# Kernel tuning notes

Measured on AMD Instinct MI355X. Metric: run time of the kernel, lower is better.

Reference implementation:

```python
import jax, jax.numpy as jnp
import numpy as np

B, L, H, NH, D, I = 2, 2048, 2048, 16, 128, 8192
EPS = 1e-6
ROPE_BASE = 10000.0


def rms_norm(x, w):
    x32 = x.astype(jnp.float32)
    n = x32 * jax.lax.rsqrt(jnp.mean(x32 * x32, axis=-1, keepdims=True) + EPS)
    return (n * w).astype(x.dtype)


def rope(x, offset):
    # x: [B, L, H, D], non-traditional (half-split) RoPE
    d = x.shape[-1]
    half = d // 2
    inv_freq = 1.0 / (ROPE_BASE ** (jnp.arange(half, dtype=jnp.float32) * 2.0 / d))
    pos = jnp.arange(x.shape[1], dtype=jnp.float32) + offset
    ang = pos[:, None] * inv_freq[None, :]              # [L, half]
    cos = jnp.cos(ang)[None, :, None, :]
    sin = jnp.sin(ang)[None, :, None, :]
    x1, x2 = x[..., :half], x[..., half:]
    out = jnp.concatenate([x1 * cos - x2 * sin, x2 * cos + x1 * sin], axis=-1)
    return out.astype(x.dtype)


def setup_inputs() -> dict:
    key = jax.random.key(0)
    ks = jax.random.split(key, 9)
    s = 0.02
    causal = jnp.where(jnp.tril(jnp.ones((L, L), dtype=bool)), 0.0, -1e9).astype(jnp.float32)
    return {
        "x": jax.random.normal(ks[0], (B, L, H), dtype=jnp.float32),
        "ln1_w": jnp.ones((H,), dtype=jnp.float32),
        "ln2_w": jnp.ones((H,), dtype=jnp.float32),
        "wq": jax.random.normal(ks[1], (H, H), dtype=jnp.float32) * s,
        "wk": jax.random.normal(ks[2], (H, H), dtype=jnp.float32) * s,
        "wv": jax.random.normal(ks[3], (H, H), dtype=jnp.float32) * s,
        "wo": jax.random.normal(ks[4], (H, H), dtype=jnp.float32) * s,
        "w_gate": jax.random.normal(ks[5], (I, H), dtype=jnp.float32) * s,
        "w_up": jax.random.normal(ks[6], (I, H), dtype=jnp.float32) * s,
        "w_down": jax.random.normal(ks[7], (H, I), dtype=jnp.float32) * s,
        "mask": causal,
        "offset": 0,
    }


def reference(x, ln1_w, ln2_w, wq, wk, wv, wo, w_gate, w_up, w_down, mask, offset):
    residual = x
    h = rms_norm(x, ln1_w)
    # QKV projections (torch Linear: y = x @ W.T)
    q = jnp.einsum("ble,oe->blo", h, wq).reshape(B, L, NH, D)
    k = jnp.einsum("ble,oe->blo", h, wk).reshape(B, L, NH, D)
    v = jnp.einsum("ble,oe->blo", h, wv).reshape(B, L, NH, D)
    q = rope(q, offset)
    k = rope(k, offset)
    # [B, NH, L, D]
    q = q.transpose(0, 2, 1, 3)
    k = k.transpose(0, 2, 1, 3)
    v = v.transpose(0, 2, 1, 3)
    scores = jnp.einsum("bhqd,bhkd->bhqk", q.astype(jnp.float32), k.astype(jnp.float32))
    scores = scores / np.sqrt(D).astype(np.float32)
    if mask is not None:
        scores = scores + mask
    probs = jax.nn.softmax(scores, axis=-1).astype(v.dtype)
    attn = jnp.einsum("bhqk,bhkd->bhqd", probs, v)
    attn = attn.transpose(0, 2, 1, 3).reshape(B, L, NH * D)
    h = jnp.einsum("blo,eo->ble", attn, wo)
    x = h + residual
    residual = x
    h = rms_norm(x, ln2_w)
    gate = jax.nn.silu(jnp.einsum("ble,ie->bli", h, w_gate))
    up = jnp.einsum("ble,ie->bli", h, w_up)
    mlp = jnp.einsum("bli,ei->ble", gate * up, w_down)
    return mlp + residual
```

## Files before the change

kernel.cpp:

```cpp
#include <hip/hip_runtime.h>
#include <stdint.h>

#define B_ 2
#define L_ 2048
#define H_ 2048
#define NH_ 16
#define D_ 128
#define I_ 8192
#define M_ (B_*L_)

typedef unsigned short u16;
typedef __attribute__((ext_vector_type(8))) short bf16x8;
typedef __attribute__((ext_vector_type(4))) float f32x4;

__device__ __forceinline__ u16 f2bf(float f) {
  union { float f; uint32_t u; } c; c.f = f;
  return (u16)((c.u + 0x7fffu + ((c.u >> 16) & 1u)) >> 16);
}
__device__ __forceinline__ float bf2f(u16 h) {
  union { uint32_t u; float f; } c; c.u = ((uint32_t)h) << 16;
  return c.f;
}
__device__ __forceinline__ void gload16(const void* g, void* l) {
  __builtin_amdgcn_global_load_lds(
      (__attribute__((address_space(1))) void*)g,
      (__attribute__((address_space(3))) void*)l, 16, 0, 0);
}

__global__ void cvt_w(const float* __restrict__ src, u16* __restrict__ dst, int n4) {
  int i = blockIdx.x * blockDim.x + threadIdx.x;
  if (i >= n4) return;
  float4 v = ((const float4*)src)[i];
  ushort4 o;
  o.x = f2bf(v.x); o.y = f2bf(v.y); o.z = f2bf(v.z); o.w = f2bf(v.w);
  ((ushort4*)dst)[i] = o;
}

__global__ __launch_bounds__(256) void rmsnorm_k(const float* __restrict__ x,
                                                 const float* __restrict__ w,
                                                 u16* __restrict__ out) {
  int row = blockIdx.x;
  int t = threadIdx.x;
  const float4* xr = (const float4*)(x + (size_t)row * H_);
  float4 a = xr[t * 2], b = xr[t * 2 + 1];
  float s = a.x*a.x + a.y*a.y + a.z*a.z + a.w*a.w
          + b.x*b.x + b.y*b.y + b.z*b.z + b.w*b.w;
  for (int m = 1; m < 64; m <<= 1) s += __shfl_xor(s, m);
  __shared__ float sm[4];
  if ((t & 63) == 0) sm[t >> 6] = s;
  __syncthreads();
  float tot = sm[0] + sm[1] + sm[2] + sm[3];
  float rs = rsqrtf(tot / (float)H_ + 1e-6f);
  const float4* wr = (const float4*)w;
  float4 w0 = wr[t * 2], w1 = wr[t * 2 + 1];
  ushort4 o0, o1;
  o0.x = f2bf(a.x * rs * w0.x); o0.y = f2bf(a.y * rs * w0.y);
  o0.z = f2bf(a.z * rs * w0.z); o0.w = f2bf(a.w * rs * w0.w);
  o1.x = f2bf(b.x * rs * w1.x); o1.y = f2bf(b.y * rs * w1.y);
  o1.z = f2bf(b.z * rs * w1.z); o1.w = f2bf(b.w * rs * w1.w);
  ushort4* orow = (ushort4*)(out + (size_t)row * H_);
  orow[t * 2] = o0; orow[t * 2 + 1] = o1;
}

__global__ void rope_tab(float* __restrict__ cosT, float* __restrict__ sinT,
                         const int* __restrict__ offp) {
  int i = blockIdx.x * blockDim.x + threadIdx.x;
  int d = i & 63, l = i >> 6;
  float inv = powf(10000.0f, -(float)d / 64.0f);
  float ang = (float)(l + *offp) * inv;
  cosT[i] = cosf(ang);
  sinT[i] = sinf(ang);
}

__global__ void rope_apply(u16* __restrict__ qk, const float* __restrict__ cosT,
                           const float* __restrict__ sinT) {
  int i = blockIdx.x * blockDim.x + threadIdx.x;
  int d = i & 63;
  size_t row = (size_t)(i >> 6);
  int l = (int)(row & (L_ - 1));
  u16* p = qk + row * D_;
  float x1 = bf2f(p[d]), x2 = bf2f(p[d + 64]);
  float c = cosT[l * 64 + d], s = sinT[l * 64 + d];
  p[d]      = f2bf(x1 * c - x2 * s);
  p[d + 64] = f2bf(x2 * c + x1 * s);
}

__global__ __launch_bounds__(256) void vtrans_k(const u16* __restrict__ v,
                                                u16* __restrict__ vt) {
  __shared__ u16 tile[64][65];
  int l0 = blockIdx.x * 64, d0 = blockIdx.y * 64;
  size_t base = (size_t)blockIdx.z * L_ * D_;
  int t = threadIdx.x;
  int tr = t >> 3, tc = (t & 7) * 8;
  #pragma unroll
  for (int it = 0; it < 2; ++it) {
    int r = tr + it * 32;
    const u16* src = v + base + (size_t)(l0 + r) * D_ + d0 + tc;
    ushort4 u0 = ((const ushort4*)src)[0], u1 = ((const ushort4*)src)[1];
    tile[r][tc + 0] = u0.x; tile[r][tc + 1] = u0.y;
    tile[r][tc + 2] = u0.z; tile[r][tc + 3] = u0.w;
    tile[r][tc + 4] = u1.x; tile[r][tc + 5] = u1.y;
    tile[r][tc + 6] = u1.z; tile[r][tc + 7] = u1.w;
  }
  __syncthreads();
  #pragma unroll
  for (int it = 0; it < 2; ++it) {
    int r = tr + it * 32;
    u16* dst = vt + base + (size_t)(d0 + r) * L_ + l0 + tc;
    ushort4 o0, o1;
    o0.x = tile[tc + 0][r]; o0.y = tile[tc + 1][r];
    o0.z = tile[tc + 2][r]; o0.w = tile[tc + 3][r];
    o1.x = tile[tc + 4][r]; o1.y = tile[tc + 5][r];
    o1.z = tile[tc + 6][r]; o1.w = tile[tc + 7][r];
    ((ushort4*)dst)[0] = o0; ((ushort4*)dst)[1] = o1;
  }
}

#define EPI_QKV 0
#define EPI_SILU 1
#define EPI_MUL 2
#define EPI_ADDRES 3

template <int EPI>
__global__ __launch_bounds__(256)
void gemm_bt(const u16* __restrict__ A, const u16* __restrict__ Bw,
             int M, int N, int K,
             u16* outb, float* outf, const float* __restrict__ resf) {
  __shared__ __attribute__((aligned(16))) u16 At[128 * 64];
  __shared__ __attribute__((aligned(16))) u16 Bt[128 * 64];
  int tid = threadIdx.x;
  int w = tid >> 6, lane = tid & 63;
  int r16 = lane & 15, g4 = lane >> 4;
  int wr = w >> 1, wc = w & 1;
  int m0 = blockIdx.y * 128;
  int n0 = blockIdx.x * 128;
  f32x4 acc[4][4] = {};
  const char* Ab = (const char*)A;
  const char* Bb = (const char*)Bw;
  int nk = K >> 6;
  for (int kt = 0; kt < nk; ++kt) {
    int k0 = kt << 6;
    #pragma unroll
    for (int i = 0; i < 4; ++i) {
      int uoff = i * 4096 + w * 1024;
      int lin = uoff + lane * 16;
      int row = lin >> 7;
      int colB = lin & 127;
      gload16(Ab + ((size_t)(m0 + row) * K + k0) * 2 + colB, (char*)At + uoff);
      gload16(Bb + ((size_t)(n0 + row) * K + k0) * 2 + colB, (char*)Bt + uoff);
    }
    __syncthreads();
    #pragma unroll
    for (int kk = 0; kk < 2; ++kk) {
      bf16x8 af[4], bfr[4];
      #pragma unroll
      for (int m = 0; m < 4; ++m)
        af[m] = *(const bf16x8*)&At[(wr * 64 + m * 16 + r16) * 64 + kk * 32 + g4 * 8];
      #pragma unroll
      for (int n = 0; n < 4; ++n)
        bfr[n] = *(const bf16x8*)&Bt[(wc * 64 + n * 16 + r16) * 64 + kk * 32 + g4 * 8];
      #pragma unroll
      for (int m = 0; m < 4; ++m)
        #pragma unroll
        for (int n = 0; n < 4; ++n)
          acc[m][n] = __builtin_amdgcn_mfma_f32_16x16x32_bf16(af[m], bfr[n], acc[m][n], 0, 0, 0);
    }
    __syncthreads();
  }
  #pragma unroll
  for (int m = 0; m < 4; ++m) {
    #pragma unroll
    for (int n = 0; n < 4; ++n) {
      #pragma unroll
      for (int r = 0; r < 4; ++r) {
        int row = m0 + wr * 64 + m * 16 + g4 * 4 + r;
        int col = n0 + wc * 64 + n * 16 + r16;
        float val = acc[m][n][r];
        if (EPI == EPI_QKV) {
          int b = row >> 11, l = row & 2047;
          int hh = col >> 7, d = col & 127;
          outb[((((size_t)b * NH_ + hh) * L_ + l) << 7) + d] = f2bf(val);
        } else if (EPI == EPI_SILU) {
          float sg = val / (1.0f + __expf(-val));
          outb[(size_t)row * N + col] = f2bf(sg);
        } else if (EPI == EPI_MUL) {
          float g = bf2f(outb[(size_t)row * N + col]);
          outb[(size_t)row * N + col] = f2bf(g * val);
        } else {
          outf[(size_t)row * N + col] = val + resf[(size_t)row * N + col];
        }
      }
    }
  }
}

template <int EPI>
__global__ __launch_bounds__(512, 2)
void gemm256(const u16* __restrict__ A, const u16* __restrict__ Bw,
             int M, int N, int K, u16* __restrict__ outb) {
  __shared__ __attribute__((aligned(16))) u16 Asm[2][2][8192];
  __shared__ __attribute__((aligned(16))) u16 Bsm[2][2][8192];
  int tid = threadIdx.x;
  int wid = tid >> 6, lane = tid & 63;
  int r16 = lane & 15, g4 = lane >> 4;
  int nwg = gridDim.x, bid = blockIdx.x;
  int q8 = nwg >> 3, r8 = nwg & 7, xcd = bid & 7, loc = bid >> 3;
  int wg = (xcd < r8 ? xcd * (q8 + 1) : r8 * (q8 + 1) + (xcd - r8) * q8) + loc;
  int NX = N >> 8;
  int n0 = (wg % NX) * 256;
  int m0 = (wg / NX) * 256;
  const char* Ab = (const char*)A;
  const char* Bb = (const char*)Bw;
  int nk = K >> 6;

  f32x4 acc[2][2][4][2] = {};
  bf16x8 afr[4][2];
  bf16x8 bfr[2][2][2];

  auto STAGE = [&](int kt1, int sel) {
    if (kt1 >= nk) return;
    int buf = kt1 & 1;
    int k0 = kt1 << 6;
    const char* gb; char* lb; int row0;
    if (sel == 0)      { gb = Ab; row0 = m0;       lb = (char*)&Asm[buf][0][0]; }
    else if (sel == 3) { gb = Ab; row0 = m0 + 128; lb = (char*)&Asm[buf][1][0]; }
    else if (sel == 1) { gb = Bb; row0 = n0;       lb = (char*)&Bsm[buf][0][0]; }
    else               { gb = Bb; row0 = n0 + 128; lb = (char*)&Bsm[buf][1][0]; }
    #pragma unroll
    for (int j = 0; j < 2; ++j) {
      int p = j * 8192 + wid * 1024 + lane * 16;
      int r = p >> 7;
      int cb = (p & 127) ^ ((r & 7) << 4);
      gload16(gb + ((size_t)(row0 + r) * K + k0) * 2 + cb,
              lb + j * 8192 + wid * 1024);
    }
  };

  STAGE(0, 0); STAGE(0, 1); STAGE(0, 2); STAGE(0, 3);

  const int QM[4] = {0, 0, 1, 1};
  const int QN[4] = {0, 1, 1, 0};

  for (int kt = 0; kt < nk; ++kt) {
    int cur = kt & 1;
    #pragma unroll
    for (int ph = 0; ph < 4; ++ph) {
      if (ph < 3) {
        __builtin_amdgcn_sched_barrier(0);
        asm volatile("s_waitcnt vmcnt(4)" ::: "memory");
      }
      __builtin_amdgcn_s_barrier();
      __builtin_amdgcn_sched_barrier(0);
      const int qm = QM[ph], qn = QN[ph];
      if (ph == 0 || ph == 2) {
        const char* Ah = (const char*)&Asm[cur][qm][0];
        #pragma unroll
        for (int mf = 0; mf < 4; ++mf) {
          int R = (wid >> 2) * 64 + mf * 16 + r16;
          int sw = (R & 7) << 4;
          afr[mf][0] = *(const bf16x8*)(Ah + R * 128 + ((g4 * 16) ^ sw));
          afr[mf][1] = *(const bf16x8*)(Ah + R * 128 + ((64 + g4 * 16) ^ sw));
        }
      }
      if (ph == 0 || ph == 1) {
        const char* Bh = (const char*)&Bsm[cur][qn][0];
        #pragma unroll
        for (int nf = 0; nf < 2; ++nf) {
          int R = (wid & 3) * 32 + nf * 16 + r16;
          int sw = (R & 7) << 4;
          bfr[qn][nf][0] = *(const bf16x8*)(Bh + R * 128 + ((g4 * 16) ^ sw));
          bfr[qn][nf][1] = *(const bf16x8*)(Bh + R * 128 + ((64 + g4 * 16) ^ sw));
        }
      }
      STAGE(kt + 1, ph);
      __builtin_amdgcn_s_setprio(1);
      #pragma unroll
      for (int mf = 0; mf < 4; ++mf)
        #pragma unroll
        for (int nf = 0; nf < 2; ++nf)
          #pragma unroll
          for (int kk = 0; kk < 2; ++kk)
            acc[qm][qn][mf][nf] = __builtin_amdgcn_mfma_f32_16x16x32_bf16(
                afr[mf][kk], bfr[qn][nf][kk], acc[qm][qn][mf][nf], 0, 0, 0);
      __builtin_amdgcn_s_setprio(0);
    }
  }
  #pragma unroll
  for (int qm = 0; qm < 2; ++qm)
    #pragma unroll
    for (int qn = 0; qn < 2; ++qn)
      #pragma unroll
      for (int mf = 0; mf < 4; ++mf)
        #pragma unroll
        for (int nf = 0; nf < 2; ++nf)
          #pragma unroll
          for (int rr = 0; rr < 4; ++rr) {
            int row = m0 + qm * 128 + (wid >> 2) * 64 + mf * 16 + g4 * 4 + rr;
            int col = n0 + qn * 128 + (wid & 3) * 32 + nf * 16 + r16;
            float val = acc[qm][qn][mf][nf][rr];
            if (EPI == EPI_SILU) {
              outb[(size_t)row * N + col] = f2bf(val / (1.0f + __expf(-val)));
            } else {
              float g = bf2f(outb[(size_t)row * N + col]);
              outb[(size_t)row * N + col] = f2bf(g * val);
            }
          }
}

__global__ __launch_bounds__(256)
void flash_attn(const u16* __restrict__ q, const u16* __restrict__ k,
                const u16* __restrict__ vt, u16* __restrict__ out) {
  __shared__ __attribute__((aligned(16))) u16 Kt[64 * 128];
  __shared__ __attribute__((aligned(16))) u16 Vt[128 * 64];
  __shared__ __attribute__((aligned(16))) u16 Pl[4][16 * 64];
  int tid = threadIdx.x, w = tid >> 6, lane = tid & 63;
  int r16 = lane & 15, g4 = lane >> 4;
  int b = blockIdx.z, h = blockIdx.y;
  int qt = gridDim.x - 1 - blockIdx.x;
  int q0 = qt * 64;
  size_t bh = (size_t)b * NH_ + h;
  const char* qb = (const char*)(q + bh * L_ * D_);
  const char* kb = (const char*)(k + bh * L_ * D_);
  const char* vb = (const char*)(vt + bh * D_ * L_);
  int qrow = q0 + w * 16 + r16;
  bf16x8 qf[4];
  #pragma unroll
  for (int c = 0; c < 4; ++c)
    qf[c] = *(const bf16x8*)(qb + ((size_t)qrow * 128 + c * 32 + g4 * 8) * 2);
  f32x4 oacc[8] = {};
  float mrow[4], lsum[4];
  #pragma unroll
  for (int r = 0; r < 4; ++r) { mrow[r] = -3.0e38f; lsum[r] = 0.f; }
  int myq = q0 + w * 16 + g4 * 4;
  int ntiles = qt + 1;
  int rsw = (r16 & 7) << 4;
  const float sc = 0.08838834764831845f;
  for (int t = 0; t < ntiles; ++t) {
    int kv0 = t * 64;
    #pragma unroll
    for (int i = 0; i < 4; ++i) {
      int uoff = i * 4096 + w * 1024;
      int lin = uoff + lane * 16;
      int krow = lin >> 8;
      int kcol = (lin & 255) ^ ((krow & 7) << 4);
      gload16(kb + (size_t)(kv0 + krow) * 256 + kcol, (char*)Kt + uoff);
      int vrow = lin >> 7;
      int vcol = (lin & 127) ^ ((vrow & 7) << 4);
      gload16(vb + (size_t)vrow * (L_ * 2) + kv0 * 2 + vcol, (char*)Vt + uoff);
    }
    __syncthreads();
    f32x4 s[4] = {};
    __builtin_amdgcn_s_setprio(1);
    #pragma unroll
    for (int c = 0; c < 4; ++c) {
      #pragma unroll
      for (int n = 0; n < 4; ++n) {
        const char* kp = (const char*)Kt + (n * 16 + r16) * 256
                       + ((c * 64 + g4 * 16) ^ rsw);
        bf16x8 kf = *(const bf16x8*)kp;
        s[n] = __builtin_amdgcn_mfma_f32_16x16x32_bf16(qf[c], kf, s[n], 0, 0, 0);
      }
    }
    __builtin_amdgcn_s_setprio(0);
    #pragma unroll
    for (int r = 0; r < 4; ++r) {
      float rm = -3.0e38f;
      #pragma unroll
      for (int n = 0; n < 4; ++n) {
        float v = s[n][r] * sc;
        int kvi = kv0 + n * 16 + r16;
        if (kvi > myq + r) v = -3.0e38f;
        s[n][r] = v;
        rm = fmaxf(rm, v);
      }
      rm = fmaxf(rm, __shfl_xor(rm, 1));
      rm = fmaxf(rm, __shfl_xor(rm, 2));
      rm = fmaxf(rm, __shfl_xor(rm, 4));
      rm = fmaxf(rm, __shfl_xor(rm, 8));
      float mnew = fmaxf(mrow[r], rm);
      float alpha = __expf(mrow[r] - mnew);
      mrow[r] = mnew;
      lsum[r] *= alpha;
      #pragma unroll
      for (int nf = 0; nf < 8; ++nf) oacc[nf][r] *= alpha;
      int prow = g4 * 4 + r;
      int psw = (prow & 7) << 3;
      #pragma unroll
      for (int n = 0; n < 4; ++n) {
        float pv = __expf(s[n][r] - mnew);
        lsum[r] += pv;
        Pl[w][prow * 64 + ((n * 16 + r16) ^ psw)] = f2bf(pv);
      }
    }
    asm volatile("s_waitcnt lgkmcnt(0)" ::: "memory");
    __builtin_amdgcn_sched_barrier(0);
    __builtin_amdgcn_s_setprio(1);
    #pragma unroll
    for (int kc = 0; kc < 2; ++kc) {
      const char* pp = (const char*)&Pl[w][0] + r16 * 128
                     + ((kc * 64 + g4 * 16) ^ rsw);
      bf16x8 pf = *(const bf16x8*)pp;
      #pragma unroll
      for (int nf = 0; nf < 8; ++nf) {
        const char* vp = (const char*)Vt + (nf * 16 + r16) * 128
                       + ((kc * 64 + g4 * 16) ^ rsw);
        bf16x8 vf = *(const bf16x8*)vp;
        oacc[nf] = __builtin_amdgcn_mfma_f32_16x16x32_bf16(pf, vf, oacc[nf], 0, 0, 0);
      }
    }
    __builtin_amdgcn_s_setprio(0);
    __syncthreads();
  }
  #pragma unroll
  for (int r = 0; r < 4; ++r) {
    float l = lsum[r];
    l += __shfl_xor(l, 1); l += __shfl_xor(l, 2);
    l += __shfl_xor(l, 4); l += __shfl_xor(l, 8);
    float inv = 1.0f / l;
    size_t orow = ((size_t)b * L_ + (myq + r)) * H_ + h * D_;
    #pragma unroll
    for (int nf = 0; nf < 8; ++nf)
      out[orow + nf * 16 + r16] = f2bf(oacc[nf][r] * inv);
  }
}

extern "C" void kernel_launch(void* const* d_in, const int* in_sizes, int n_in,
                              void* d_out, int out_size, void* d_ws, size_t ws_size,
                              hipStream_t stream) {
  (void)in_sizes; (void)n_in; (void)out_size; (void)ws_size;
  const float* x    = (const float*)d_in[0];
  const float* ln1w = (const float*)d_in[1];
  const float* ln2w = (const float*)d_in[2];
  const float* wq   = (const float*)d_in[3];
  const float* wk   = (const float*)d_in[4];
  const float* wv   = (const float*)d_in[5];
  const float* wo   = (const float*)d_in[6];
  const float* wg   = (const float*)d_in[7];
  const float* wu   = (const float*)d_in[8];
  const float* wd   = (const float*)d_in[9];
  const int*   offp = (const int*)d_in[11];
  float* out = (float*)d_out;

  char* p = (char*)d_ws;
  auto alloc = [&](size_t bytes) {
    char* r = p;
    p += (bytes + 255) & ~(size_t)255;
    return r;
  };
  const size_t HH = (size_t)H_ * H_, IH = (size_t)I_ * H_;
  u16* wbuf = (u16*)alloc(IH * 2);
  u16* h1   = (u16*)alloc((size_t)M_ * H_ * 2);
  u16* qb   = (u16*)alloc((size_t)M_ * H_ * 2);
  u16* kb   = (u16*)alloc((size_t)M_ * H_ * 2);
  u16* vb   = (u16*)alloc((size_t)M_ * H_ * 2);
  u16* vtb  = (u16*)alloc((size_t)M_ * H_ * 2);
  u16* attn = (u16*)alloc((size_t)M_ * H_ * 2);
  float* x2 = (float*)alloc((size_t)M_ * H_ * 4);
  float* cosT = (float*)alloc((size_t)L_ * 64 * 4);
  float* sinT = (float*)alloc((size_t)L_ * 64 * 4);
  u16* h2    = h1;
  u16* gateb = qb;

  const int nHH4 = (int)(HH / 4), nIH4 = (int)(IH / 4);

  rmsnorm_k<<<M_, 256, 0, stream>>>(x, ln1w, h1);
  rope_tab<<<(L_ * 64) / 256, 256, 0, stream>>>(cosT, sinT, offp);

  dim3 g1(H_ / 128, M_ / 128);
  cvt_w<<<nHH4 / 256, 256, 0, stream>>>(wq, wbuf, nHH4);
  gemm_bt<EPI_QKV><<<g1, 256, 0, stream>>>(h1, wbuf, M_, H_, H_, qb, nullptr, nullptr);
  cvt_w<<<nHH4 / 256, 256, 0, stream>>>(wk, wbuf, nHH4);
  gemm_bt<EPI_QKV><<<g1, 256, 0, stream>>>(h1, wbuf, M_, H_, H_, kb, nullptr, nullptr);
  cvt_w<<<nHH4 / 256, 256, 0, stream>>>(wv, wbuf, nHH4);
  gemm_bt<EPI_QKV><<<g1, 256, 0, stream>>>(h1, wbuf, M_, H_, H_, vb, nullptr, nullptr);

  int nrope = B_ * NH_ * L_ * 64;
  rope_apply<<<nrope / 256, 256, 0, stream>>>(qb, cosT, sinT);
  rope_apply<<<nrope / 256, 256, 0, stream>>>(kb, cosT, sinT);
  vtrans_k<<<dim3(L_ / 64, D_ / 64, B_ * NH_), 256, 0, stream>>>(vb, vtb);

  flash_attn<<<dim3(L_ / 64, NH_, B_), 256, 0, stream>>>(qb, kb, vtb, attn);

  cvt_w<<<nHH4 / 256, 256, 0, stream>>>(wo, wbuf, nHH4);
  gemm_bt<EPI_ADDRES><<<g1, 256, 0, stream>>>(attn, wbuf, M_, H_, H_, nullptr, x2, x);
  rmsnorm_k<<<M_, 256, 0, stream>>>(x2, ln2w, h2);

  int nwg256 = (M_ / 256) * (I_ / 256);
  cvt_w<<<nIH4 / 256, 256, 0, stream>>>(wg, wbuf, nIH4);
  gemm256<EPI_SILU><<<nwg256, 512, 0, stream>>>(h2, wbuf, M_, I_, H_, gateb);
  cvt_w<<<nIH4 / 256, 256, 0, stream>>>(wu, wbuf, nIH4);
  gemm256<EPI_MUL><<<nwg256, 512, 0, stream>>>(h2, wbuf, M_, I_, H_, gateb);

  dim3 g3(H_ / 128, M_ / 128);
  cvt_w<<<nIH4 / 256, 256, 0, stream>>>(wd, wbuf, nIH4);
  gemm_bt<EPI_ADDRES><<<g3, 256, 0, stream>>>(gateb, wbuf, M_, H_, I_, nullptr, out, x2);
}
```

Baseline: 972.2 us.

## Fuse QKV into one 256-tile GEMM and split-K the down projection

The three separate Q/K/V 128-tile GEMMs are replaced by one 256-tile GEMM over a concatenated 3H weight buffer, with an epilogue that scatters into head-major Q/K/V slices. The down projection moves from the 128-tile kernel to the 256-tile kernel with split-K=2. Each half writes bf16 partials that a new reduce kernel sums with the residual. This is meant to raise tile efficiency and occupancy for GEMMs whose 256-tile grid would otherwise be too small. In exchange it adds extra partial traffic, rounds the partial sums to bf16, and adds one more launch.

```diff
diff --git a/kernel.cpp b/kernel.cpp
--- a/kernel.cpp
+++ b/kernel.cpp
@@ -34,6 +34,23 @@
   ushort4 o;
   o.x = f2bf(v.x); o.y = f2bf(v.y); o.z = f2bf(v.z); o.w = f2bf(v.w);
   ((ushort4*)dst)[i] = o;
+}
+
+__global__ __launch_bounds__(256) void down_reduce(const u16* __restrict__ p0,
+                                                   const u16* __restrict__ p1,
+                                                   const float* __restrict__ res,
+                                                   float* __restrict__ out, int n4) {
+  int i = blockIdx.x * blockDim.x + threadIdx.x;
+  if (i >= n4) return;
+  ushort4 a = ((const ushort4*)p0)[i];
+  ushort4 b = ((const ushort4*)p1)[i];
+  float4 r = ((const float4*)res)[i];
+  float4 o;
+  o.x = bf2f(a.x) + bf2f(b.x) + r.x;
+  o.y = bf2f(a.y) + bf2f(b.y) + r.y;
+  o.z = bf2f(a.z) + bf2f(b.z) + r.z;
+  o.w = bf2f(a.w) + bf2f(b.w) + r.w;
+  ((float4*)out)[i] = o;
 }
 
 __global__ __launch_bounds__(256) void rmsnorm_k(const float* __restrict__ x,
@@ -120,6 +137,8 @@
 #define EPI_SILU 1
 #define EPI_MUL 2
 #define EPI_ADDRES 3
+#define EPI_PART 4
+#define EPI_QKV3 5
 
 template <int EPI>
 __global__ __launch_bounds__(256)
@@ -197,7 +216,8 @@
 template <int EPI>
 __global__ __launch_bounds__(512, 2)
 void gemm256(const u16* __restrict__ A, const u16* __restrict__ Bw,
-             int M, int N, int K, u16* __restrict__ outb) {
+             int M, int N, int K, int nk, int nslice,
+             u16* __restrict__ outb, u16* __restrict__ outb2) {
   __shared__ __attribute__((aligned(16))) u16 Asm[2][2][8192];
   __shared__ __attribute__((aligned(16))) u16 Bsm[2][2][8192];
   int tid = threadIdx.x;
@@ -205,13 +225,17 @@
   int r16 = lane & 15, g4 = lane >> 4;
   int nwg = gridDim.x, bid = blockIdx.x;
   int q8 = nwg >> 3, r8 = nwg & 7, xcd = bid & 7, loc = bid >> 3;
-  int wg = (xcd < r8 ? xcd * (q8 + 1) : r8 * (q8 + 1) + (xcd - r8) * q8) + loc;
+  int wgall = (xcd < r8 ? xcd * (q8 + 1) : r8 * (q8 + 1) + (xcd - r8) * q8) + loc;
+  int nwg_geo = (M >> 8) * (N >> 8);
+  int ks = wgall / nwg_geo;
+  int wg = wgall % nwg_geo;
+  (void)nslice;
   int NX = N >> 8;
   int n0 = (wg % NX) * 256;
   int m0 = (wg / NX) * 256;
-  const char* Ab = (const char*)A;
-  const char* Bb = (const char*)Bw;
-  int nk = K >> 6;
+  const char* Ab = (const char*)(A + (size_t)ks * nk * 64);
+  const char* Bb = (const char*)(Bw + (size_t)ks * nk * 64);
+  u16* ob = (EPI == EPI_PART && ks) ? outb2 : outb;
 
   f32x4 acc[2][2][4][2] = {};
   bf16x8 afr[4][2];
@@ -299,10 +323,18 @@
             int col = n0 + qn * 128 + (wid & 3) * 32 + nf * 16 + r16;
             float val = acc[qm][qn][mf][nf][rr];
             if (EPI == EPI_SILU) {
-              outb[(size_t)row * N + col] = f2bf(val / (1.0f + __expf(-val)));
-            } else {
-              float g = bf2f(outb[(size_t)row * N + col]);
-              outb[(size_t)row * N + col] = f2bf(g * val);
+              ob[(size_t)row * N + col] = f2bf(val / (1.0f + __expf(-val)));
+            } else if (EPI == EPI_MUL) {
+              float g = bf2f(ob[(size_t)row * N + col]);
+              ob[(size_t)row * N + col] = f2bf(g * val);
+            } else if (EPI == EPI_PART) {
+              ob[(size_t)row * N + col] = f2bf(val);
+            } else if (EPI == EPI_QKV3) {
+              int which = col >> 11, within = col & 2047;
+              int hh = within >> 7, d = within & 127;
+              int bb = row >> 11, l = row & 2047;
+              ob[(size_t)which * M_ * H_ +
+                 ((((size_t)bb * NH_ + hh) * L_ + l) << 7) + d] = f2bf(val);
             }
           }
 }
@@ -458,6 +490,7 @@
   float* x2 = (float*)alloc((size_t)M_ * H_ * 4);
   float* cosT = (float*)alloc((size_t)L_ * 64 * 4);
   float* sinT = (float*)alloc((size_t)L_ * 64 * 4);
+  (void)kb; (void)vb;
   u16* h2    = h1;
   u16* gateb = qb;
 
@@ -466,32 +499,39 @@
   rmsnorm_k<<<M_, 256, 0, stream>>>(x, ln1w, h1);
   rope_tab<<<(L_ * 64) / 256, 256, 0, stream>>>(cosT, sinT, offp);
 
-  dim3 g1(H_ / 128, M_ / 128);
   cvt_w<<<nHH4 / 256, 256, 0, stream>>>(wq, wbuf, nHH4);
-  gemm_bt<EPI_QKV><<<g1, 256, 0, stream>>>(h1, wbuf, M_, H_, H_, qb, nullptr, nullptr);
-  cvt_w<<<nHH4 / 256, 256, 0, stream>>>(wk, wbuf, nHH4);
-  gemm_bt<EPI_QKV><<<g1, 256, 0, stream>>>(h1, wbuf, M_, H_, H_, kb, nullptr, nullptr);
-  cvt_w<<<nHH4 / 256, 256, 0, stream>>>(wv, wbuf, nHH4);
-  gemm_bt<EPI_QKV><<<g1, 256, 0, stream>>>(h1, wbuf, M_, H_, H_, vb, nullptr, nullptr);
+  cvt_w<<<nHH4 / 256, 256, 0, stream>>>(wk, wbuf + HH, nHH4);
+  cvt_w<<<nHH4 / 256, 256, 0, stream>>>(wv, wbuf + 2 * HH, nHH4);
+  int nwg_qkv = (M_ / 256) * (3 * H_ / 256);
+  gemm256<EPI_QKV3><<<nwg_qkv, 512, 0, stream>>>(h1, wbuf, M_, 3 * H_, H_,
+                                                 H_ / 64, 1, qb, nullptr);
 
   int nrope = B_ * NH_ * L_ * 64;
   rope_apply<<<nrope / 256, 256, 0, stream>>>(qb, cosT, sinT);
-  rope_apply<<<nrope / 256, 256, 0, stream>>>(kb, cosT, sinT);
-  vtrans_k<<<dim3(L_ / 64, D_ / 64, B_ * NH_), 256, 0, stream>>>(vb, vtb);
-
-  flash_attn<<<dim3(L_ / 64, NH_, B_), 256, 0, stream>>>(qb, kb, vtb, attn);
-
+  rope_apply<<<nrope / 256, 256, 0, stream>>>(qb + (size_t)M_ * H_, cosT, sinT);
+  vtrans_k<<<dim3(L_ / 64, D_ / 64, B_ * NH_), 256, 0, stream>>>(
+      qb + 2 * (size_t)M_ * H_, vtb);
+
+  flash_attn<<<dim3(L_ / 64, NH_, B_), 256, 0, stream>>>(
+      qb, qb + (size_t)M_ * H_, vtb, attn);
+
+  dim3 g1(H_ / 128, M_ / 128);
   cvt_w<<<nHH4 / 256, 256, 0, stream>>>(wo, wbuf, nHH4);
   gemm_bt<EPI_ADDRES><<<g1, 256, 0, stream>>>(attn, wbuf, M_, H_, H_, nullptr, x2, x);
   rmsnorm_k<<<M_, 256, 0, stream>>>(x2, ln2w, h2);
 
   int nwg256 = (M_ / 256) * (I_ / 256);
   cvt_w<<<nIH4 / 256, 256, 0, stream>>>(wg, wbuf, nIH4);
-  gemm256<EPI_SILU><<<nwg256, 512, 0, stream>>>(h2, wbuf, M_, I_, H_, gateb);
+  gemm256<EPI_SILU><<<nwg256, 512, 0, stream>>>(h2, wbuf, M_, I_, H_,
+                                                H_ / 64, 1, gateb, nullptr);
   cvt_w<<<nIH4 / 256, 256, 0, stream>>>(wu, wbuf, nIH4);
-  gemm256<EPI_MUL><<<nwg256, 512, 0, stream>>>(h2, wbuf, M_, I_, H_, gateb);
-
-  dim3 g3(H_ / 128, M_ / 128);
+  gemm256<EPI_MUL><<<nwg256, 512, 0, stream>>>(h2, wbuf, M_, I_, H_,
+                                               H_ / 64, 1, gateb, nullptr);
+
   cvt_w<<<nIH4 / 256, 256, 0, stream>>>(wd, wbuf, nIH4);
-  gemm_bt<EPI_ADDRES><<<g3, 256, 0, stream>>>(gateb, wbuf, M_, H_, I_, nullptr, out, x2);
-}
+  int nwg_dn = 2 * (M_ / 256) * (H_ / 256);
+  gemm256<EPI_PART><<<nwg_dn, 512, 0, stream>>>(gateb, wbuf, M_, H_, I_,
+                                                I_ / 128, 2, h1, attn);
+  down_reduce<<<(M_ * H_ / 4) / 256, 256, 0, stream>>>(h1, attn, x2, out,
+                                                       M_ * H_ / 4);
+}
```

Result: faster. 868.9 us (-10.6%).
